# Performance work log

Measured on AMD Instinct MI355X. Metric: run time of the kernel, lower is better.

The kernel has to match this reference:

```python
import jax, jax.numpy as jnp
import numpy as np

B, C, H, W = 16, 512, 32, 32
EPS = 1e-5

def setup_inputs() -> dict:
    key = jax.random.key(0)
    ks = jax.random.split(key, 7)
    s = 1.0 / np.sqrt(C)
    return {
        "x": jax.random.normal(ks[0], (B, C, H, W), dtype=jnp.float32),
        "norm_w": jnp.ones((C,), jnp.float32),
        "norm_b": jnp.zeros((C,), jnp.float32),
        "qkv_w": jax.random.normal(ks[1], (3 * C, C), dtype=jnp.float32) * s,
        "qkv_b": jax.random.normal(ks[2], (3 * C,), dtype=jnp.float32) * 0.01,
        "out_w": jax.random.normal(ks[3], (C, C), dtype=jnp.float32) * s,
        "out_b": jax.random.normal(ks[4], (C,), dtype=jnp.float32) * 0.01,
    }

def reference(x, norm_w, norm_b, qkv_w, qkv_b, out_w, out_b):
    b, c, h, w = x.shape
    # GroupNorm with num_groups=1: normalize over (C,H,W) per sample, per-channel affine
    mean = jnp.mean(x, axis=(1, 2, 3), keepdims=True)
    var = jnp.var(x, axis=(1, 2, 3), keepdims=True)
    xn = (x - mean) * jax.lax.rsqrt(var + EPS)
    xn = xn * norm_w[None, :, None, None] + norm_b[None, :, None, None]
    # 1x1 conv QKV: [b,3c,h,w]
    qkv = jnp.einsum('bchw,oc->bohw', xn, qkv_w) + qkv_b[None, :, None, None]
    q, k, v = jnp.split(qkv, 3, axis=1)
    n = h * w
    q = q.transpose(0, 2, 3, 1).reshape(b, n, c)   # [b, N, c]
    k = k.reshape(b, c, n)                          # [b, c, N]
    v = v.transpose(0, 2, 3, 1).reshape(b, n, c)   # [b, N, c]
    scores = jnp.einsum('bnc,bcm->bnm', q, k) * (c ** -0.5)  # [b, N, N]
    attn = jax.nn.softmax(scores, axis=-1)
    out = jnp.einsum('bnm,bmc->bnc', attn, v)       # [b, N, c]
    out = out.reshape(b, h, w, c).transpose(0, 3, 1, 2)
    out = jnp.einsum('bchw,oc->bohw', out, out_w) + out_b[None, :, None, None]
    return out + x
```

## Files before the change

kernel.cpp:

```cpp
#include <hip/hip_runtime.h>
#include <math.h>

#define BATCH 16
#define CH    512
#define NTOK  1024
#define CHW   (CH * NTOK)
#define EPSV  1e-5f

typedef __attribute__((ext_vector_type(8))) short bf16x8;
typedef __attribute__((ext_vector_type(4))) float f32x4;

__device__ __forceinline__ unsigned short f2bf(float f) {
    union { float f; unsigned u; } cv; cv.f = f;
    unsigned r = cv.u + 0x7FFFu + ((cv.u >> 16) & 1u);
    return (unsigned short)(r >> 16);
}
__device__ __forceinline__ float bf2f(unsigned short u) {
    union { unsigned u; float f; } cv; cv.u = ((unsigned)u) << 16;
    return cv.f;
}

__device__ __forceinline__ void async16(const unsigned short* g, unsigned short* l) {
    __builtin_amdgcn_global_load_lds(
        (const __attribute__((address_space(1))) void*)g,
        (__attribute__((address_space(3))) void*)l,
        16, 0, 0);
}

static const size_t OFF_WQKV = 256;
static const size_t OFF_OW   = OFF_WQKV + 1572864;
static const size_t OFF_XNT  = OFF_OW   + 524288;
static const size_t OFF_QT   = OFF_XNT  + 16777216;
static const size_t OFF_KT   = OFF_QT   + 16777216;
static const size_t OFF_V    = OFF_KT   + 16777216;
static const size_t OFF_OT   = OFF_V    + 16777216;
static const size_t OFF_S    = OFF_OT   + 16777216;
static const size_t OFF_P    = OFF_S    + 33554432;

__global__ void k_zero_stats(float* ws) {
    if (threadIdx.x < 64) ws[threadIdx.x] = 0.0f;
}

__global__ __launch_bounds__(256) void k_stats_partial(const float* __restrict__ x, float* __restrict__ ws) {
    int blk   = blockIdx.x;
    int b     = blk >> 6;
    int chunk = blk & 63;
    const float4* xp = (const float4*)(x + (size_t)b * CHW + (size_t)chunk * 8192);
    int t = threadIdx.x;
    float s = 0.0f, ss = 0.0f;
#pragma unroll
    for (int j = 0; j < 8; j++) {
        float4 v = xp[t + j * 256];
        s  += v.x + v.y + v.z + v.w;
        ss += v.x * v.x + v.y * v.y + v.z * v.z + v.w * v.w;
    }
#pragma unroll
    for (int off = 32; off; off >>= 1) {
        s  += __shfl_xor(s, off, 64);
        ss += __shfl_xor(ss, off, 64);
    }
    __shared__ float ls[4], lss[4];
    int wave = t >> 6, lane = t & 63;
    if (lane == 0) { ls[wave] = s; lss[wave] = ss; }
    __syncthreads();
    if (t == 0) {
        atomicAdd(&ws[b], ls[0] + ls[1] + ls[2] + ls[3]);
        atomicAdd(&ws[16 + b], lss[0] + lss[1] + lss[2] + lss[3]);
    }
}

__global__ void k_stats_final(float* ws) {
    int b = threadIdx.x;
    if (b < 16) {
        float inv  = 1.0f / (float)CHW;
        float mean = ws[b] * inv;
        float var  = ws[16 + b] * inv - mean * mean;
        ws[32 + b] = mean;
        ws[48 + b] = rsqrtf(var + EPSV);
    }
}

__global__ __launch_bounds__(256) void k_cvt(const float* __restrict__ in, unsigned short* __restrict__ out, int n4) {
    int i = blockIdx.x * 256 + threadIdx.x;
    if (i < n4) {
        float4 v = ((const float4*)in)[i];
        ushort4 o;
        o.x = f2bf(v.x); o.y = f2bf(v.y); o.z = f2bf(v.z); o.w = f2bf(v.w);
        ((ushort4*)out)[i] = o;
    }
}

__global__ __launch_bounds__(256) void k_xnt(const float* __restrict__ x,
                                             const float* __restrict__ nw,
                                             const float* __restrict__ nb,
                                             const float* __restrict__ ws,
                                             unsigned short* __restrict__ xnt) {
    __shared__ float ls[64][65];
    int b  = blockIdx.z;
    int c0 = blockIdx.y * 64;
    int n0 = blockIdx.x * 64;
    float mean = ws[32 + b], rstd = ws[48 + b];
    int t = threadIdx.x;
    int cl = t >> 4, n4 = t & 15;
    const float* xb = x + (size_t)b * CHW;
#pragma unroll
    for (int i = 0; i < 4; i++) {
        int c = c0 + cl + i * 16;
        float a  = rstd * nw[c];
        float bb = nb[c] - mean * a;
        float4 v = *(const float4*)(xb + (size_t)c * NTOK + n0 + n4 * 4);
        ls[cl + i * 16][n4 * 4 + 0] = v.x * a + bb;
        ls[cl + i * 16][n4 * 4 + 1] = v.y * a + bb;
        ls[cl + i * 16][n4 * 4 + 2] = v.z * a + bb;
        ls[cl + i * 16][n4 * 4 + 3] = v.w * a + bb;
    }
    __syncthreads();
    int nl = t >> 4, c4 = t & 15;
    unsigned short* dst = xnt + (size_t)b * NTOK * CH;
#pragma unroll
    for (int i = 0; i < 4; i++) {
        int n = n0 + nl + i * 16;
        ushort4 o;
        o.x = f2bf(ls[c4 * 4 + 0][nl + i * 16]);
        o.y = f2bf(ls[c4 * 4 + 1][nl + i * 16]);
        o.z = f2bf(ls[c4 * 4 + 2][nl + i * 16]);
        o.w = f2bf(ls[c4 * 4 + 3][nl + i * 16]);
        *(ushort4*)(dst + (size_t)n * CH + c0 + c4 * 4) = o;
    }
}

__device__ __forceinline__ void mfma_core(const unsigned short* __restrict__ A, int lda,
                                          const unsigned short* __restrict__ B, int ldb,
                                          int K, int m0, int n0,
                                          unsigned short* sA, unsigned short* sB,
                                          f32x4 acc[4][4]) {
    const int t = threadIdx.x;
    const int w = t >> 6, lane = t & 63;
    const int wm = (w & 1) * 64, wn = (w >> 1) * 64;
    const int r16 = lane & 15, quad = lane >> 4;
#pragma unroll
    for (int i = 0; i < 4; i++)
#pragma unroll
        for (int j = 0; j < 4; j++) acc[i][j] = (f32x4){0.f, 0.f, 0.f, 0.f};
    const int sr = lane >> 2;
    const int sk = (lane & 3) * 8;
    const unsigned short* gA0 = A + (size_t)(m0 + w * 32 + sr) * lda + sk;
    const unsigned short* gA1 = gA0 + (size_t)16 * lda;
    const unsigned short* gB0 = B + (size_t)(n0 + w * 32 + sr) * ldb + sk;
    const unsigned short* gB1 = gB0 + (size_t)16 * ldb;
    unsigned short* lA0 = sA + (w * 32)      * 32;
    unsigned short* lA1 = sA + (w * 32 + 16) * 32;
    unsigned short* lB0 = sB + (w * 32)      * 32;
    unsigned short* lB1 = sB + (w * 32 + 16) * 32;
    for (int k0 = 0; k0 < K; k0 += 32) {
        async16(gA0 + k0, lA0);
        async16(gA1 + k0, lA1);
        async16(gB0 + k0, lB0);
        async16(gB1 + k0, lB1);
        __syncthreads();
        bf16x8 af[4], bfr[4];
#pragma unroll
        for (int i = 0; i < 4; i++) af[i]  = *(const bf16x8*)(sA + (wm + i * 16 + r16) * 32 + quad * 8);
#pragma unroll
        for (int j = 0; j < 4; j++) bfr[j] = *(const bf16x8*)(sB + (wn + j * 16 + r16) * 32 + quad * 8);
#pragma unroll
        for (int i = 0; i < 4; i++)
#pragma unroll
            for (int j = 0; j < 4; j++)
                acc[i][j] = __builtin_amdgcn_mfma_f32_16x16x32_bf16(af[i], bfr[j], acc[i][j], 0, 0, 0);
        __syncthreads();
    }
}

__global__ __launch_bounds__(256) void k_gemm_qkv(const unsigned short* __restrict__ Wq,
                                                  const float* __restrict__ qb,
                                                  const unsigned short* __restrict__ XNT,
                                                  unsigned short* __restrict__ QT,
                                                  unsigned short* __restrict__ KT,
                                                  unsigned short* __restrict__ V) {
    __shared__ __align__(16) unsigned short sA[128 * 32];
    __shared__ __align__(16) unsigned short sB[128 * 32];
    const int b  = blockIdx.z;
    const int m0 = blockIdx.y * 128;
    const int n0 = blockIdx.x * 128;
    f32x4 acc[4][4];
    mfma_core(Wq, CH, XNT + (size_t)b * NTOK * CH, CH, CH, m0, n0, sA, sB, acc);
    const int t = threadIdx.x;
    const int w = t >> 6, lane = t & 63;
    const int wm = (w & 1) * 64, wn = (w >> 1) * 64;
    const int r16 = lane & 15, quad = lane >> 4;
    const int region = m0 >> 9;
    unsigned short* dstT = (region == 0) ? QT : KT;
#pragma unroll
    for (int i = 0; i < 4; i++) {
        const int o0g = m0 + wm + i * 16 + quad * 4;
        const int ro  = o0g & 511;
#pragma unroll
        for (int j = 0; j < 4; j++) {
            const int col = n0 + wn + j * 16 + r16;
            f32x4 a = acc[i][j];
            if (region < 2) {
                ushort4 pk;
                pk.x = f2bf(a[0] + qb[o0g + 0]);
                pk.y = f2bf(a[1] + qb[o0g + 1]);
                pk.z = f2bf(a[2] + qb[o0g + 2]);
                pk.w = f2bf(a[3] + qb[o0g + 3]);
                *(ushort4*)(dstT + (size_t)b * NTOK * CH + (size_t)col * CH + ro) = pk;
            } else {
#pragma unroll
                for (int r = 0; r < 4; r++)
                    V[(size_t)b * CH * NTOK + (size_t)(ro + r) * NTOK + col] = f2bf(a[r] + qb[o0g + r]);
            }
        }
    }
}

__global__ __launch_bounds__(256) void k_gemm_sc(const unsigned short* __restrict__ QT,
                                                 const unsigned short* __restrict__ KT,
                                                 unsigned short* __restrict__ S) {
    __shared__ __align__(16) unsigned short sA[128 * 32];
    __shared__ __align__(16) unsigned short sB[128 * 32];
    const int b  = blockIdx.z;
    const int m0 = blockIdx.y * 128;
    const int n0 = blockIdx.x * 128;
    f32x4 acc[4][4];
    mfma_core(QT + (size_t)b * NTOK * CH, CH, KT + (size_t)b * NTOK * CH, CH, CH, m0, n0, sA, sB, acc);
    const int t = threadIdx.x;
    const int w = t >> 6, lane = t & 63;
    const int wm = (w & 1) * 64, wn = (w >> 1) * 64;
    const int r16 = lane & 15, quad = lane >> 4;
    const float scale = 0.044194173824159216f;
    unsigned short* Sb = S + (size_t)b * NTOK * NTOK;
#pragma unroll
    for (int i = 0; i < 4; i++) {
        const int row0 = m0 + wm + i * 16 + quad * 4;
#pragma unroll
        for (int j = 0; j < 4; j++) {
            const int col = n0 + wn + j * 16 + r16;
            f32x4 a = acc[i][j];
#pragma unroll
            for (int r = 0; r < 4; r++)
                Sb[(size_t)(row0 + r) * NTOK + col] = f2bf(a[r] * scale);
        }
    }
}

__global__ __launch_bounds__(256) void k_softmax(const unsigned short* __restrict__ S, unsigned short* __restrict__ P) {
    size_t row = blockIdx.x;
    const unsigned short* p = S + row * NTOK;
    unsigned short* q = P + row * NTOK;
    int t = threadIdx.x;
    int wave = t >> 6, lane = t & 63;
    __shared__ float red[4];
    ushort4 u = ((const ushort4*)p)[t];
    float4 v;
    v.x = bf2f(u.x); v.y = bf2f(u.y); v.z = bf2f(u.z); v.w = bf2f(u.w);
    float m = fmaxf(fmaxf(v.x, v.y), fmaxf(v.z, v.w));
#pragma unroll
    for (int off = 32; off; off >>= 1) m = fmaxf(m, __shfl_xor(m, off, 64));
    if (lane == 0) red[wave] = m;
    __syncthreads();
    m = fmaxf(fmaxf(red[0], red[1]), fmaxf(red[2], red[3]));
    __syncthreads();
    v.x = __expf(v.x - m);
    v.y = __expf(v.y - m);
    v.z = __expf(v.z - m);
    v.w = __expf(v.w - m);
    float s = v.x + v.y + v.z + v.w;
#pragma unroll
    for (int off = 32; off; off >>= 1) s += __shfl_xor(s, off, 64);
    if (lane == 0) red[wave] = s;
    __syncthreads();
    s = red[0] + red[1] + red[2] + red[3];
    float inv = 1.0f / s;
    ushort4 o;
    o.x = f2bf(v.x * inv); o.y = f2bf(v.y * inv); o.z = f2bf(v.z * inv); o.w = f2bf(v.w * inv);
    ((ushort4*)q)[t] = o;
}

__global__ __launch_bounds__(256) void k_gemm_av(const unsigned short* __restrict__ V,
                                                 const unsigned short* __restrict__ P,
                                                 unsigned short* __restrict__ OT) {
    __shared__ __align__(16) unsigned short sA[128 * 32];
    __shared__ __align__(16) unsigned short sB[128 * 32];
    const int b  = blockIdx.z;
    const int m0 = blockIdx.y * 128;
    const int n0 = blockIdx.x * 128;
    f32x4 acc[4][4];
    mfma_core(V + (size_t)b * CH * NTOK, NTOK, P + (size_t)b * NTOK * NTOK, NTOK, NTOK, m0, n0, sA, sB, acc);
    const int t = threadIdx.x;
    const int w = t >> 6, lane = t & 63;
    const int wm = (w & 1) * 64, wn = (w >> 1) * 64;
    const int r16 = lane & 15, quad = lane >> 4;
    unsigned short* OTb = OT + (size_t)b * NTOK * CH;
#pragma unroll
    for (int i = 0; i < 4; i++) {
        const int c0g = m0 + wm + i * 16 + quad * 4;
#pragma unroll
        for (int j = 0; j < 4; j++) {
            const int col = n0 + wn + j * 16 + r16;
            f32x4 a = acc[i][j];
            ushort4 pk;
            pk.x = f2bf(a[0]); pk.y = f2bf(a[1]); pk.z = f2bf(a[2]); pk.w = f2bf(a[3]);
            *(ushort4*)(OTb + (size_t)col * CH + c0g) = pk;
        }
    }
}

__global__ __launch_bounds__(256) void k_gemm_out(const unsigned short* __restrict__ OW,
                                                  const float* __restrict__ ob,
                                                  const unsigned short* __restrict__ OT,
                                                  const float* __restrict__ x,
                                                  float* __restrict__ out) {
    __shared__ __align__(16) unsigned short sA[128 * 32];
    __shared__ __align__(16) unsigned short sB[128 * 32];
    const int b  = blockIdx.z;
    const int m0 = blockIdx.y * 128;
    const int n0 = blockIdx.x * 128;
    f32x4 acc[4][4];
    mfma_core(OW, CH, OT + (size_t)b * NTOK * CH, CH, CH, m0, n0, sA, sB, acc);
    const int t = threadIdx.x;
    const int w = t >> 6, lane = t & 63;
    const int wm = (w & 1) * 64, wn = (w >> 1) * 64;
    const int r16 = lane & 15, quad = lane >> 4;
#pragma unroll
    for (int i = 0; i < 4; i++) {
        const int o0g = m0 + wm + i * 16 + quad * 4;
#pragma unroll
        for (int j = 0; j < 4; j++) {
            const int col = n0 + wn + j * 16 + r16;
            f32x4 a = acc[i][j];
#pragma unroll
            for (int r = 0; r < 4; r++) {
                size_t idx = (size_t)b * CHW + (size_t)(o0g + r) * NTOK + col;
                out[idx] = a[r] + ob[o0g + r] + x[idx];
            }
        }
    }
}

extern "C" void kernel_launch(void* const* d_in, const int* in_sizes, int n_in,
                              void* d_out, int out_size, void* d_ws, size_t ws_size,
                              hipStream_t stream) {
    const float* x      = (const float*)d_in[0];
    const float* norm_w = (const float*)d_in[1];
    const float* norm_b = (const float*)d_in[2];
    const float* qkv_w  = (const float*)d_in[3];
    const float* qkv_b  = (const float*)d_in[4];
    const float* out_w  = (const float*)d_in[5];
    const float* out_b  = (const float*)d_in[6];
    float* out = (float*)d_out;
    char* wsb  = (char*)d_ws;

    float* stats = (float*)wsb;
    unsigned short* WQ  = (unsigned short*)(wsb + OFF_WQKV);
    unsigned short* OW  = (unsigned short*)(wsb + OFF_OW);
    unsigned short* XNT = (unsigned short*)(wsb + OFF_XNT);
    unsigned short* QT  = (unsigned short*)(wsb + OFF_QT);
    unsigned short* KT  = (unsigned short*)(wsb + OFF_KT);
    unsigned short* V   = (unsigned short*)(wsb + OFF_V);
    unsigned short* OT  = (unsigned short*)(wsb + OFF_OT);
    unsigned short* S   = (unsigned short*)(wsb + OFF_S);
    unsigned short* P   = (unsigned short*)(wsb + OFF_P);

    k_zero_stats<<<1, 64, 0, stream>>>(stats);
    k_stats_partial<<<BATCH * 64, 256, 0, stream>>>(x, stats);
    k_stats_final<<<1, 16, 0, stream>>>(stats);
    k_cvt<<<768, 256, 0, stream>>>(qkv_w, WQ, 3 * CH * CH / 4);
    k_cvt<<<256, 256, 0, stream>>>(out_w, OW, CH * CH / 4);
    k_xnt<<<dim3(NTOK / 64, CH / 64, BATCH), 256, 0, stream>>>(x, norm_w, norm_b, stats, XNT);
    k_gemm_qkv<<<dim3(NTOK / 128, 3 * CH / 128, BATCH), 256, 0, stream>>>(WQ, qkv_b, XNT, QT, KT, V);
    k_gemm_sc<<<dim3(NTOK / 128, NTOK / 128, BATCH), 256, 0, stream>>>(QT, KT, S);
    k_softmax<<<BATCH * NTOK, 256, 0, stream>>>(S, P);
    k_gemm_av<<<dim3(NTOK / 128, CH / 128, BATCH), 256, 0, stream>>>(V, P, OT);
    k_gemm_out<<<dim3(NTOK / 128, CH / 128, BATCH), 256, 0, stream>>>(OW, out_b, OT, x, out);
}
```

Before: 266.2 us.

## Double-buffer GEMM LDS tiles and stage transposed epilogues through shared memory

The shared MFMA mainloop now ping-pongs between two LDS buffers, prefetching the next K tile while computing the current one, and drops one barrier per iteration. The QKV and AV GEMM epilogues write results into a padded LDS tile first, then emit coalesced row stores, instead of strided or 2-byte scattered global writes. This aims to hide global load latency and improve store coalescing. The cost is doubled shared-memory use, which may lower occupancy, plus extra barriers and LDS traffic in the epilogue.

```diff
diff --git a/kernel.cpp b/kernel.cpp
--- a/kernel.cpp
+++ b/kernel.cpp
@@ -132,7 +132,7 @@
 __device__ __forceinline__ void mfma_core(const unsigned short* __restrict__ A, int lda,
                                           const unsigned short* __restrict__ B, int ldb,
                                           int K, int m0, int n0,
-                                          unsigned short* sA, unsigned short* sB,
+                                          unsigned short* sm,
                                           f32x4 acc[4][4]) {
     const int t = threadIdx.x;
     const int w = t >> 6, lane = t & 63;
@@ -148,29 +148,40 @@
     const unsigned short* gA1 = gA0 + (size_t)16 * lda;
     const unsigned short* gB0 = B + (size_t)(n0 + w * 32 + sr) * ldb + sk;
     const unsigned short* gB1 = gB0 + (size_t)16 * ldb;
-    unsigned short* lA0 = sA + (w * 32)      * 32;
-    unsigned short* lA1 = sA + (w * 32 + 16) * 32;
-    unsigned short* lB0 = sB + (w * 32)      * 32;
-    unsigned short* lB1 = sB + (w * 32 + 16) * 32;
-    for (int k0 = 0; k0 < K; k0 += 32) {
-        async16(gA0 + k0, lA0);
-        async16(gA1 + k0, lA1);
-        async16(gB0 + k0, lB0);
-        async16(gB1 + k0, lB1);
+    unsigned short* lA0 = sm + (w * 32) * 32;
+    unsigned short* lA1 = sm + (w * 32 + 16) * 32;
+    unsigned short* lB0 = sm + 8192 + (w * 32) * 32;
+    unsigned short* lB1 = sm + 8192 + (w * 32 + 16) * 32;
+    const int T = K >> 5;
+    async16(gA0, lA0);
+    async16(gA1, lA1);
+    async16(gB0, lB0);
+    async16(gB1, lB1);
+    for (int tt = 0; tt < T; tt++) {
         __syncthreads();
+        const int cur = (tt & 1) << 12;
+        if (tt + 1 < T) {
+            const int nxt = cur ^ 4096;
+            const int ko = (tt + 1) << 5;
+            async16(gA0 + ko, lA0 + nxt);
+            async16(gA1 + ko, lA1 + nxt);
+            async16(gB0 + ko, lB0 + nxt);
+            async16(gB1 + ko, lB1 + nxt);
+        }
         bf16x8 af[4], bfr[4];
 #pragma unroll
-        for (int i = 0; i < 4; i++) af[i]  = *(const bf16x8*)(sA + (wm + i * 16 + r16) * 32 + quad * 8);
-#pragma unroll
-        for (int j = 0; j < 4; j++) bfr[j] = *(const bf16x8*)(sB + (wn + j * 16 + r16) * 32 + quad * 8);
+        for (int i = 0; i < 4; i++) af[i]  = *(const bf16x8*)(sm + cur + (wm + i * 16 + r16) * 32 + quad * 8);
+#pragma unroll
+        for (int j = 0; j < 4; j++) bfr[j] = *(const bf16x8*)(sm + 8192 + cur + (wn + j * 16 + r16) * 32 + quad * 8);
 #pragma unroll
         for (int i = 0; i < 4; i++)
 #pragma unroll
             for (int j = 0; j < 4; j++)
                 acc[i][j] = __builtin_amdgcn_mfma_f32_16x16x32_bf16(af[i], bfr[j], acc[i][j], 0, 0, 0);
-        __syncthreads();
-    }
-}
+    }
+}
+
+#define TSTRIDE 136
 
 __global__ __launch_bounds__(256) void k_gemm_qkv(const unsigned short* __restrict__ Wq,
                                                   const float* __restrict__ qb,
@@ -178,39 +189,63 @@
                                                   unsigned short* __restrict__ QT,
                                                   unsigned short* __restrict__ KT,
                                                   unsigned short* __restrict__ V) {
-    __shared__ __align__(16) unsigned short sA[128 * 32];
-    __shared__ __align__(16) unsigned short sB[128 * 32];
+    __shared__ __align__(16) unsigned short smem[128 * TSTRIDE];
     const int b  = blockIdx.z;
     const int m0 = blockIdx.y * 128;
     const int n0 = blockIdx.x * 128;
     f32x4 acc[4][4];
-    mfma_core(Wq, CH, XNT + (size_t)b * NTOK * CH, CH, CH, m0, n0, sA, sB, acc);
+    mfma_core(Wq, CH, XNT + (size_t)b * NTOK * CH, CH, CH, m0, n0, smem, acc);
     const int t = threadIdx.x;
     const int w = t >> 6, lane = t & 63;
     const int wm = (w & 1) * 64, wn = (w >> 1) * 64;
     const int r16 = lane & 15, quad = lane >> 4;
     const int region = m0 >> 9;
-    unsigned short* dstT = (region == 0) ? QT : KT;
-#pragma unroll
-    for (int i = 0; i < 4; i++) {
-        const int o0g = m0 + wm + i * 16 + quad * 4;
-        const int ro  = o0g & 511;
-#pragma unroll
-        for (int j = 0; j < 4; j++) {
-            const int col = n0 + wn + j * 16 + r16;
-            f32x4 a = acc[i][j];
-            if (region < 2) {
+    __syncthreads();
+    if (region < 2) {
+#pragma unroll
+        for (int i = 0; i < 4; i++) {
+            const int ol = wm + i * 16 + quad * 4;
+            const int og = m0 + ol;
+            const float b0 = qb[og], b1 = qb[og + 1], b2 = qb[og + 2], b3 = qb[og + 3];
+#pragma unroll
+            for (int j = 0; j < 4; j++) {
+                const int nl = wn + j * 16 + r16;
+                f32x4 a = acc[i][j];
                 ushort4 pk;
-                pk.x = f2bf(a[0] + qb[o0g + 0]);
-                pk.y = f2bf(a[1] + qb[o0g + 1]);
-                pk.z = f2bf(a[2] + qb[o0g + 2]);
-                pk.w = f2bf(a[3] + qb[o0g + 3]);
-                *(ushort4*)(dstT + (size_t)b * NTOK * CH + (size_t)col * CH + ro) = pk;
-            } else {
+                pk.x = f2bf(a[0] + b0); pk.y = f2bf(a[1] + b1);
+                pk.z = f2bf(a[2] + b2); pk.w = f2bf(a[3] + b3);
+                *(ushort4*)(smem + nl * TSTRIDE + ol) = pk;
+            }
+        }
+        __syncthreads();
+        unsigned short* dst = ((region == 0) ? QT : KT) + (size_t)b * NTOK * CH + (size_t)n0 * CH + (m0 & 511);
+#pragma unroll
+        for (int p = 0; p < 16; p++) {
+            const int row = (t >> 5) + p * 8;
+            const int seg = (t & 31) * 4;
+            *(ushort4*)(dst + (size_t)row * CH + seg) = *(const ushort4*)(smem + row * TSTRIDE + seg);
+        }
+    } else {
+#pragma unroll
+        for (int i = 0; i < 4; i++) {
+            const int ol = wm + i * 16 + quad * 4;
+            const int og = m0 + ol;
+#pragma unroll
+            for (int j = 0; j < 4; j++) {
+                const int nl = wn + j * 16 + r16;
+                f32x4 a = acc[i][j];
 #pragma unroll
                 for (int r = 0; r < 4; r++)
-                    V[(size_t)b * CH * NTOK + (size_t)(ro + r) * NTOK + col] = f2bf(a[r] + qb[o0g + r]);
+                    smem[(ol + r) * TSTRIDE + nl] = f2bf(a[r] + qb[og + r]);
             }
+        }
+        __syncthreads();
+        unsigned short* dst = V + (size_t)b * CH * NTOK + (size_t)(m0 & 511) * NTOK + n0;
+#pragma unroll
+        for (int p = 0; p < 16; p++) {
+            const int row = (t >> 5) + p * 8;
+            const int seg = (t & 31) * 4;
+            *(ushort4*)(dst + (size_t)row * NTOK + seg) = *(const ushort4*)(smem + row * TSTRIDE + seg);
         }
     }
 }
@@ -218,13 +253,12 @@
 __global__ __launch_bounds__(256) void k_gemm_sc(const unsigned short* __restrict__ QT,
                                                  const unsigned short* __restrict__ KT,
                                                  unsigned short* __restrict__ S) {
-    __shared__ __align__(16) unsigned short sA[128 * 32];
-    __shared__ __align__(16) unsigned short sB[128 * 32];
+    __shared__ __align__(16) unsigned short smem[16384];
     const int b  = blockIdx.z;
     const int m0 = blockIdx.y * 128;
     const int n0 = blockIdx.x * 128;
     f32x4 acc[4][4];
-    mfma_core(QT + (size_t)b * NTOK * CH, CH, KT + (size_t)b * NTOK * CH, CH, CH, m0, n0, sA, sB, acc);
+    mfma_core(QT + (size_t)b * NTOK * CH, CH, KT + (size_t)b * NTOK * CH, CH, CH, m0, n0, smem, acc);
     const int t = threadIdx.x;
     const int w = t >> 6, lane = t & 63;
     const int wm = (w & 1) * 64, wn = (w >> 1) * 64;
@@ -281,29 +315,36 @@
 __global__ __launch_bounds__(256) void k_gemm_av(const unsigned short* __restrict__ V,
                                                  const unsigned short* __restrict__ P,
                                                  unsigned short* __restrict__ OT) {
-    __shared__ __align__(16) unsigned short sA[128 * 32];
-    __shared__ __align__(16) unsigned short sB[128 * 32];
+    __shared__ __align__(16) unsigned short smem[128 * TSTRIDE];
     const int b  = blockIdx.z;
     const int m0 = blockIdx.y * 128;
     const int n0 = blockIdx.x * 128;
     f32x4 acc[4][4];
-    mfma_core(V + (size_t)b * CH * NTOK, NTOK, P + (size_t)b * NTOK * NTOK, NTOK, NTOK, m0, n0, sA, sB, acc);
+    mfma_core(V + (size_t)b * CH * NTOK, NTOK, P + (size_t)b * NTOK * NTOK, NTOK, NTOK, m0, n0, smem, acc);
     const int t = threadIdx.x;
     const int w = t >> 6, lane = t & 63;
     const int wm = (w & 1) * 64, wn = (w >> 1) * 64;
     const int r16 = lane & 15, quad = lane >> 4;
-    unsigned short* OTb = OT + (size_t)b * NTOK * CH;
+    __syncthreads();
 #pragma unroll
     for (int i = 0; i < 4; i++) {
-        const int c0g = m0 + wm + i * 16 + quad * 4;
+        const int cl = wm + i * 16 + quad * 4;
 #pragma unroll
         for (int j = 0; j < 4; j++) {
-            const int col = n0 + wn + j * 16 + r16;
+            const int nl = wn + j * 16 + r16;
             f32x4 a = acc[i][j];
             ushort4 pk;
             pk.x = f2bf(a[0]); pk.y = f2bf(a[1]); pk.z = f2bf(a[2]); pk.w = f2bf(a[3]);
-            *(ushort4*)(OTb + (size_t)col * CH + c0g) = pk;
-        }
+            *(ushort4*)(smem + nl * TSTRIDE + cl) = pk;
+        }
+    }
+    __syncthreads();
+    unsigned short* dst = OT + (size_t)b * NTOK * CH + (size_t)n0 * CH + m0;
+#pragma unroll
+    for (int p = 0; p < 16; p++) {
+        const int row = (t >> 5) + p * 8;
+        const int seg = (t & 31) * 4;
+        *(ushort4*)(dst + (size_t)row * CH + seg) = *(const ushort4*)(smem + row * TSTRIDE + seg);
     }
 }
 
@@ -312,13 +353,12 @@
                                                   const unsigned short* __restrict__ OT,
                                                   const float* __restrict__ x,
                                                   float* __restrict__ out) {
-    __shared__ __align__(16) unsigned short sA[128 * 32];
-    __shared__ __align__(16) unsigned short sB[128 * 32];
+    __shared__ __align__(16) unsigned short smem[16384];
     const int b  = blockIdx.z;
     const int m0 = blockIdx.y * 128;
     const int n0 = blockIdx.x * 128;
     f32x4 acc[4][4];
-    mfma_core(OW, CH, OT + (size_t)b * NTOK * CH, CH, CH, m0, n0, sA, sB, acc);
+    mfma_core(OW, CH, OT + (size_t)b * NTOK * CH, CH, CH, m0, n0, smem, acc);
     const int t = threadIdx.x;
     const int w = t >> 6, lane = t & 63;
     const int wm = (w & 1) * 64, wn = (w >> 1) * 64;
```

After: 258.6 us. 2.8% less time.
